# Performance work log

Hardware: AMD Instinct MI355X
Metric: run time of the kernel (lower is better)

## Reference

```python
import jax, jax.numpy as jnp
from jax import lax
import numpy as np

B = 16384


def setup_inputs() -> dict:
    key = jax.random.key(0)
    ks = jax.random.split(key, 8)
    g = lambda k, s: jax.random.normal(k, s, jnp.float32) * 0.05
    return {
        'data': (jax.random.uniform(ks[0], (B, 10, 10, 1)) > 0.9).astype(jnp.float32),
        'w1': g(ks[1], (3, 3, 1, 128)),   'b1': jnp.zeros((128,), jnp.float32),
        'w2': g(ks[2], (3, 3, 128, 128)), 'b2': jnp.zeros((128,), jnp.float32),
        'w3': g(ks[3], (3, 3, 128, 64)),  'b3': jnp.zeros((64,), jnp.float32),
        'w4': g(ks[4], (3, 3, 64, 64)),   'b4': jnp.zeros((64,), jnp.float32),
        'wd1': g(ks[5], (64, 32)), 'bd1': jnp.zeros((32,), jnp.float32),
        'wd2': g(ks[6], (32, 4)),  'bd2': jnp.zeros((4,), jnp.float32),
    }


DN = ('NHWC', 'HWIO', 'NHWC')


def _conv(x, w, b):
    return jax.nn.relu(lax.conv_general_dilated(x, w, (1, 1), 'SAME', dimension_numbers=DN) + b)


def _pool(x):  # MaxPooling2D(pool=2, strides=2, valid)
    return lax.reduce_window(x, -jnp.inf, lax.max, (1, 2, 2, 1), (1, 2, 2, 1), 'VALID')


def reference(data, w1, b1, w2, b2, w3, b3, w4, b4, wd1, bd1, wd2, bd2):
    H = W = 10.0
    x = _pool(_conv(_conv(data, w1, b1), w2, b2))          # [B,5,5,128]
    x = _pool(_conv(_conv(x, w3, b3), w4, b4))             # [B,2,2,64]
    x = jnp.mean(x, axis=(1, 2))                           # GAP -> [B,64]
    x = jax.nn.relu(x @ wd1 + bd1)
    svg = jax.nn.sigmoid(x @ wd2 + bd2).reshape(-1, 2, 2)  # [B,2,2]
    p1 = svg[:, 0, :, None]                                # [B,2,1]
    p2 = svg[:, 1, :, None]
    t = jnp.linspace(0.0, 1.0, 5)
    pts = ((1.0 - t) * p1 + t * p2).transpose(0, 2, 1)     # [B,5,2]
    pts = pts * jnp.array([H, W], jnp.float32)
    # straight-through round
    pts = pts + lax.stop_gradient(jnp.round(pts) - pts)
    # sort by linearized position
    pos = pts[:, :, 0] * W + pts[:, :, 1]
    order = jnp.argsort(pos, axis=1)
    pts = jnp.take_along_axis(pts, order[:, :, None], axis=1)
    # dedup: keep point i if L1 distance to previous point != 0 (first always kept)
    d = jnp.sum(jnp.abs(pts[:, 1:] - pts[:, :-1]), axis=2)           # [B,4]
    d = jnp.concatenate([jnp.ones((d.shape[0], 1), d.dtype), d], 1)  # [B,5]
    keep = d != 0.0
    dest = jnp.where(keep, jnp.cumsum(keep.astype(jnp.int32), axis=1) - 1, 5)
    out = jnp.full((pts.shape[0], 6, 2), -1.0, pts.dtype)  # slot 5 = trash
    out = out.at[jnp.arange(pts.shape[0])[:, None], dest].set(pts)
    return out[:, :5]                                      # [B,5,2], padded with -1
```

## Files before the change

### kernel.cpp

```cpp
#include <hip/hip_runtime.h>
#include <hip/hip_bf16.h>
#include <math.h>

typedef float f4 __attribute__((ext_vector_type(4)));
typedef float f32x4 __attribute__((ext_vector_type(4)));
typedef __bf16 bf16x8 __attribute__((ext_vector_type(8)));
typedef unsigned int uint32x4 __attribute__((ext_vector_type(4)));

#define NT 256

__global__ void repack_w(const float* __restrict__ w1, const float* __restrict__ w2,
                         const float* __restrict__ w3, const float* __restrict__ w4,
                         __hip_bfloat16* __restrict__ ws)
{
    int tid = blockIdx.x * 256 + threadIdx.x;
    const int T2 = 147456, T3 = 73728, T4 = 36864, T1 = 4096;
    if (tid < T2) {
        int j = tid & 7, l = (tid >> 3) & 63, rest = tid >> 9;
        int n = rest & 7, kidx = rest >> 3;
        int cs = kidx & 3, tap = kidx >> 2;
        int ci = cs * 32 + ((l >> 4) << 3) + j;
        int co = (n << 4) + (l & 15);
        ws[tid] = __float2bfloat16(w2[(tap * 128 + ci) * 128 + co]);
    } else if (tid < T2 + T3) {
        int t3 = tid - T2;
        int j = t3 & 7, l = (t3 >> 3) & 63, rest = t3 >> 9;
        int n = rest & 3, kidx = rest >> 2;
        int cs = kidx & 3, tap = kidx >> 2;
        int ci = cs * 32 + ((l >> 4) << 3) + j;
        int co = (n << 4) + (l & 15);
        ws[tid] = __float2bfloat16(w3[(tap * 128 + ci) * 64 + co]);
    } else if (tid < T2 + T3 + T4) {
        int t4 = tid - T2 - T3;
        int j = t4 & 7, l = (t4 >> 3) & 63, rest = t4 >> 9;
        int n = rest & 3, ks = rest >> 2;
        int half = ks & 1, tap = ks >> 1;
        int ci = half * 32 + ((l >> 4) << 3) + j;
        int co = (n << 4) + (l & 15);
        ws[tid] = __float2bfloat16(w4[(tap * 64 + ci) * 64 + co]);
    } else if (tid < T2 + T3 + T4 + T1) {
        int t1 = tid - T2 - T3 - T4;
        int j = t1 & 7, l = (t1 >> 3) & 63, n = (t1 >> 9) & 7;
        int k = ((l >> 4) << 3) + j;
        int co = (n << 4) + (l & 15);
        float v = (k < 9) ? w1[k * 128 + co] : 0.f;
        ws[tid] = __float2bfloat16(v);
    }
}

__global__ __launch_bounds__(NT, 4)
void img2svg_fused(const float* __restrict__ data,
                   const float* __restrict__ b1, const float* __restrict__ b2,
                   const float* __restrict__ b3, const float* __restrict__ b4,
                   const float* __restrict__ wd1, const float* __restrict__ bd1,
                   const float* __restrict__ wd2, const float* __restrict__ bd2,
                   const __hip_bfloat16* __restrict__ wsb,
                   float* __restrict__ out)
{
    __shared__ __align__(16) unsigned char s_u[25856];
    __shared__ float s_in[144];
    __shared__ float s_pool4[4 * 64];
    __shared__ float s_feat[64];
    __shared__ float s_h[32];

    const int t = threadIdx.x;
    const int img = blockIdx.x;
    const int w = t >> 6;
    const int lane = t & 63;
    const int kg = lane >> 4;
    const int l15 = lane & 15;
    const int kgbase1 = kg * 1616;
    const int kgbase2 = kg * 416;

    if (t < 144) {
        int r = t / 12, c = t % 12;
        float v = 0.f;
        if (r >= 1 && r <= 10 && c >= 1 && c <= 10)
            v = data[img * 100 + (r - 1) * 10 + (c - 1)];
        s_in[t] = v;
    }
    if (t < 128)
        *(__bf16*)(s_u + (t >> 3) * 1616 + 1600 + (t & 7) * 2) = (__bf16)0.f;
    s_pool4[t] = 0.f;
    __syncthreads();

    {
        const uint32x4* pk1v = (const uint32x4*)((const __hip_bfloat16*)wsb + 258048);
        uint32x4 B0 = pk1v[((w * 2 + 0) << 6) + lane];
        uint32x4 B1 = pk1v[((w * 2 + 1) << 6) + lane];
        float bj0 = b1[(w * 2 + 0) * 16 + l15];
        float bj1 = b1[(w * 2 + 1) * 16 + l15];
        const int kb0 = (w * 2 + 0) * 2 + (l15 >> 3);
        const int kb1 = (w * 2 + 1) * 2 + (l15 >> 3);
        const int cb = (l15 & 7) * 2;

        for (int mi = 0; mi < 7; ++mi) {
            int p_raw = mi * 16 + l15;
            int p = p_raw < 100 ? p_raw : 99;
            int y = p / 10, x = p - 10 * (p / 10);
            bf16x8 A = __builtin_bit_cast(bf16x8, (uint32x4){0, 0, 0, 0});
            if (kg == 0) {
#pragma unroll
                for (int j = 0; j < 8; ++j)
                    A[j] = (__bf16)s_in[(y + j / 3) * 12 + x + j % 3];
            } else if (kg == 1) {
                A[0] = (__bf16)s_in[(y + 2) * 12 + x + 2];
            }
            f32x4 c0 = (f32x4){bj0, bj0, bj0, bj0};
            f32x4 c1 = (f32x4){bj1, bj1, bj1, bj1};
            c0 = __builtin_amdgcn_mfma_f32_16x16x32_bf16(
                A, __builtin_bit_cast(bf16x8, B0), c0, 0, 0, 0);
            c1 = __builtin_amdgcn_mfma_f32_16x16x32_bf16(
                A, __builtin_bit_cast(bf16x8, B1), c1, 0, 0, 0);
#pragma unroll
            for (int rr = 0; rr < 4; ++rr) {
                int p_out = mi * 16 + kg * 4 + rr;
                if (p_out < 100) {
                    *(__bf16*)(s_u + kb0 * 1616 + p_out * 16 + cb) =
                        (__bf16)fmaxf(c0[rr], 0.f);
                    *(__bf16*)(s_u + kb1 * 1616 + p_out * 16 + cb) =
                        (__bf16)fmaxf(c1[rr], 0.f);
                }
            }
        }
    }
    __syncthreads();

    {
        const int wm = w >> 1, wn = w & 1;
        const uint32x4* pk2v = (const uint32x4*)wsb;

        f32x4 acc[4][4];
#pragma unroll
        for (int j = 0; j < 4; ++j) {
            float bj = b2[wn * 64 + j * 16 + l15];
#pragma unroll
            for (int mi = 0; mi < 4; ++mi) acc[mi][j] = (f32x4){bj, bj, bj, bj};
        }

        int py[4], px[4];
#pragma unroll
        for (int mi = 0; mi < 4; ++mi) {
            int pos = (4 * wm + mi) * 16 + l15;
            py[mi] = pos / 10;
            px[mi] = pos - 10 * py[mi];
        }

        uint32x4 Bc[4], Bn[4];
#pragma unroll
        for (int j = 0; j < 4; ++j) Bc[j] = pk2v[((wn * 4 + j) << 6) + lane];

        for (int tap = 0; tap < 9; ++tap) {
            const int dy = tap / 3, dx = tap - 3 * (tap / 3);
            int ao[4];
#pragma unroll
            for (int mi = 0; mi < 4; ++mi) {
                int ay = py[mi] + dy - 1, ax = px[mi] + dx - 1;
                int r = ((unsigned)ay < 10u && (unsigned)ax < 10u) ? ay * 10 + ax : 100;
                ao[mi] = (r << 4) + kgbase1;
            }
#pragma unroll
            for (int cs = 0; cs < 4; ++cs) {
                int nk = tap * 4 + cs + 1;
                if (nk < 36) {
#pragma unroll
                    for (int j = 0; j < 4; ++j)
                        Bn[j] = pk2v[(((nk << 3) + wn * 4 + j) << 6) + lane];
                }
                bf16x8 A[4];
#pragma unroll
                for (int mi = 0; mi < 4; ++mi)
                    A[mi] = *(const bf16x8*)(const void*)(s_u + cs * 6464 + ao[mi]);
#pragma unroll
                for (int mi = 0; mi < 4; ++mi)
#pragma unroll
                    for (int j = 0; j < 4; ++j)
                        acc[mi][j] = __builtin_amdgcn_mfma_f32_16x16x32_bf16(
                            A[mi], __builtin_bit_cast(bf16x8, Bc[j]), acc[mi][j], 0, 0, 0);
#pragma unroll
                for (int j = 0; j < 4; ++j) Bc[j] = Bn[j];
            }
        }
        __syncthreads();

        float* p2f = (float*)s_u;
        for (int i = t; i < 3200; i += NT) p2f[i] = 0.f;
        if (t < 128)
            *(__bf16*)(s_u + 13312 + (t >> 3) * 416 + 400 + (t & 7) * 2) = (__bf16)0.f;
        if (t < 64)
            *(__bf16*)(s_u + 19968 + (t >> 3) * 416 + 400 + (t & 7) * 2) = (__bf16)0.f;
        __syncthreads();

#pragma unroll
        for (int mi = 0; mi < 4; ++mi) {
            int posb = (4 * wm + mi) * 16 + kg * 4;
#pragma unroll
            for (int j = 0; j < 4; ++j) {
                int co = wn * 64 + j * 16 + l15;
                float m01 = fmaxf(fmaxf(acc[mi][j][0], acc[mi][j][1]), 0.f);
                float m23 = fmaxf(fmaxf(acc[mi][j][2], acc[mi][j][3]), 0.f);
                if (posb < 100) {
                    int y = posb / 10, x = posb - 10 * (posb / 10);
                    atomicMax((int*)&p2f[(((y >> 1) * 5 + (x >> 1)) << 7) + co],
                              __float_as_int(m01));
                }
                int pos2 = posb + 2;
                if (pos2 < 100) {
                    int y = pos2 / 10, x = pos2 - 10 * (pos2 / 10);
                    atomicMax((int*)&p2f[(((y >> 1) * 5 + (x >> 1)) << 7) + co],
                              __float_as_int(m23));
                }
            }
        }
    }
    __syncthreads();

    {
        const float* p2f = (const float*)s_u;
        for (int i = t; i < 3200; i += NT) {
            int r = i >> 7, c = i & 127;
            float v = p2f[i];
            *(__bf16*)(s_u + 13312 + (c >> 3) * 416 + (r << 4) + (c & 7) * 2) = (__bf16)v;
        }
    }
    __syncthreads();

    {
        const int mt = w & 1, ntp = w >> 1;
        const uint32x4* pk3v = (const uint32x4*)((const __hip_bfloat16*)wsb + 147456);

        f32x4 c3[2];
#pragma unroll
        for (int j = 0; j < 2; ++j) {
            float bj = b3[ntp * 32 + j * 16 + l15];
            c3[j] = (f32x4){bj, bj, bj, bj};
        }
        int pos = mt * 16 + l15;
        int p3y = pos / 5, p3x = pos - 5 * (pos / 5);

        uint32x4 Bc[2], Bn[2];
#pragma unroll
        for (int j = 0; j < 2; ++j) Bc[j] = pk3v[((ntp * 2 + j) << 6) + lane];

        for (int tap = 0; tap < 9; ++tap) {
            const int dy = tap / 3, dx = tap - 3 * (tap / 3);
            int ay = p3y + dy - 1, ax = p3x + dx - 1;
            int r = ((unsigned)ay < 5u && (unsigned)ax < 5u) ? ay * 5 + ax : 25;
            int ao = 13312 + (r << 4) + kgbase2;
#pragma unroll
            for (int cs = 0; cs < 4; ++cs) {
                int nk = tap * 4 + cs + 1;
                if (nk < 36) {
#pragma unroll
                    for (int j = 0; j < 2; ++j)
                        Bn[j] = pk3v[(((nk << 2) + ntp * 2 + j) << 6) + lane];
                }
                bf16x8 A = *(const bf16x8*)(const void*)(s_u + cs * 1664 + ao);
#pragma unroll
                for (int j = 0; j < 2; ++j)
                    c3[j] = __builtin_amdgcn_mfma_f32_16x16x32_bf16(
                        A, __builtin_bit_cast(bf16x8, Bc[j]), c3[j], 0, 0, 0);
#pragma unroll
                for (int j = 0; j < 2; ++j) Bc[j] = Bn[j];
            }
        }
#pragma unroll
        for (int j = 0; j < 2; ++j) {
            int co = ntp * 32 + j * 16 + l15;
            int kb = co >> 3, cb = (co & 7) * 2;
#pragma unroll
            for (int rr = 0; rr < 4; ++rr) {
                int p = mt * 16 + kg * 4 + rr;
                if (p < 25)
                    *(__bf16*)(s_u + 19968 + kb * 416 + p * 16 + cb) =
                        (__bf16)fmaxf(c3[j][rr], 0.f);
            }
        }
    }
    __syncthreads();

    {
        const int nt = w;
        const uint32x4* pk4v = (const uint32x4*)((const __hip_bfloat16*)wsb + 221184);
        float bj = b4[nt * 16 + l15];
        f32x4 c4 = (f32x4){bj, bj, bj, bj};
        int py = l15 >> 2, px = l15 & 3;

        uint32x4 Bc = pk4v[(nt << 6) + lane], Bn;
        for (int ks = 0; ks < 18; ++ks) {
            if (ks < 17) Bn = pk4v[((((ks + 1) << 2) + nt) << 6) + lane];
            int half = ks & 1, tap = ks >> 1;
            int dy = tap / 3, dx = tap - 3 * (tap / 3);
            int ay = py + dy - 1, ax = px + dx - 1;
            int r = ((unsigned)ay < 5u && (unsigned)ax < 5u) ? ay * 5 + ax : 25;
            bf16x8 A = *(const bf16x8*)(const void*)(
                s_u + 19968 + (half * 4 + kg) * 416 + (r << 4));
            c4 = __builtin_amdgcn_mfma_f32_16x16x32_bf16(
                A, __builtin_bit_cast(bf16x8, Bc), c4, 0, 0, 0);
            Bc = Bn;
        }
#pragma unroll
        for (int rr = 0; rr < 4; ++rr) {
            int p = kg * 4 + rr;
            int cell = ((p >> 2) >> 1) * 2 + ((p & 3) >> 1);
            float rv = fmaxf(c4[rr], 0.f);
            atomicMax((int*)&s_pool4[cell * 64 + nt * 16 + l15], __float_as_int(rv));
        }
    }
    __syncthreads();

    if (t < 64) {
        float f = 0.25f * (s_pool4[t] + s_pool4[64 + t] + s_pool4[128 + t] + s_pool4[192 + t]);
        s_feat[t] = f;
    }
    __syncthreads();
    if (t < 32) {
        float h = bd1[t];
        for (int i = 0; i < 64; ++i) h = fmaf(s_feat[i], wd1[i * 32 + t], h);
        s_h[t] = fmaxf(h, 0.f);
    }
    __syncthreads();

    if (t == 0) {
        float v[4];
#pragma unroll
        for (int o = 0; o < 4; ++o) {
            float vv = bd2[o];
            for (int i = 0; i < 32; ++i) vv = fmaf(s_h[i], wd2[i * 4 + o], vv);
            v[o] = 1.f / (1.f + expf(-vv));
        }
        float px[5], py[5], pp[5];
#pragma unroll
        for (int k = 0; k < 5; ++k) {
            float tk = 0.25f * (float)k;
            float gx = ((1.f - tk) * v[0] + tk * v[2]) * 10.f;
            float gy = ((1.f - tk) * v[1] + tk * v[3]) * 10.f;
            px[k] = rintf(gx);
            py[k] = rintf(gy);
            pp[k] = px[k] * 10.f + py[k];
        }
#pragma unroll
        for (int pass = 0; pass < 4; ++pass)
#pragma unroll
            for (int i = 0; i < 4 - pass; ++i) {
                bool sw = pp[i] > pp[i + 1];
                float a, b;
                a = pp[i]; b = pp[i + 1]; pp[i] = sw ? b : a; pp[i + 1] = sw ? a : b;
                a = px[i]; b = px[i + 1]; px[i] = sw ? b : a; px[i + 1] = sw ? a : b;
                a = py[i]; b = py[i + 1]; py[i] = sw ? b : a; py[i + 1] = sw ? a : b;
            }
        float* op = out + img * 10;
#pragma unroll
        for (int i = 0; i < 5; ++i) { op[2 * i] = -1.f; op[2 * i + 1] = -1.f; }
        int k2 = 0;
#pragma unroll
        for (int i = 0; i < 5; ++i) {
            bool keep;
            if (i == 0) keep = true;
            else keep = (fabsf(px[i] - px[i - 1]) + fabsf(py[i] - py[i - 1])) != 0.f;
            if (keep) {
                op[2 * k2] = px[i];
                op[2 * k2 + 1] = py[i];
                ++k2;
            }
        }
    }
}

extern "C" void kernel_launch(void* const* d_in, const int* in_sizes, int n_in,
                              void* d_out, int out_size, void* d_ws, size_t ws_size,
                              hipStream_t stream) {
    const float* data = (const float*)d_in[0];
    const float* w1  = (const float*)d_in[1];
    const float* b1  = (const float*)d_in[2];
    const float* w2  = (const float*)d_in[3];
    const float* b2  = (const float*)d_in[4];
    const float* w3  = (const float*)d_in[5];
    const float* b3  = (const float*)d_in[6];
    const float* w4  = (const float*)d_in[7];
    const float* b4  = (const float*)d_in[8];
    const float* wd1 = (const float*)d_in[9];
    const float* bd1 = (const float*)d_in[10];
    const float* wd2 = (const float*)d_in[11];
    const float* bd2 = (const float*)d_in[12];
    float* out = (float*)d_out;
    __hip_bfloat16* wsb = (__hip_bfloat16*)d_ws;

    repack_w<<<1024, 256, 0, stream>>>(w1, w2, w3, w4, wsb);

    int nimg = in_sizes[0] / 100;
    img2svg_fused<<<nimg, NT, 0, stream>>>(data, b1, b2, b3, b4,
                                           wd1, bd1, wd2, bd2, wsb, out);
}
```

Baseline: 675.0 us.

## Repartition conv2 waves over output channels and replace pooling atomics with two-stage max

Conv2 now splits work so each wave owns 32 output channels across all 7 position tiles, where before waves used a 2x2 split over positions and channels. Each weight fragment is loaded once per k-step per wave, and the register prefetch double-buffer is dropped. The 2x2 max-pool no longer zero-inits shared memory and uses atomicMax. Horizontal pairs are maxed in registers and written plainly, and the vertical max is fused into the bf16 transpose pass. Shared memory grows to hold the unpooled row buffer, which may lower occupancy, and the loss of weight prefetch may expose global load latency.

```diff
diff --git a/kernel.cpp b/kernel.cpp
--- a/kernel.cpp
+++ b/kernel.cpp
@@ -57,7 +57,7 @@
                    const __hip_bfloat16* __restrict__ wsb,
                    float* __restrict__ out)
 {
-    __shared__ __align__(16) unsigned char s_u[25856];
+    __shared__ __align__(16) unsigned char s_u[32256];
     __shared__ float s_in[144];
     __shared__ float s_pool4[4 * 64];
     __shared__ float s_feat[64];
@@ -127,105 +127,87 @@
     __syncthreads();
 
     {
-        const int wm = w >> 1, wn = w & 1;
         const uint32x4* pk2v = (const uint32x4*)wsb;
 
-        f32x4 acc[4][4];
-#pragma unroll
-        for (int j = 0; j < 4; ++j) {
-            float bj = b2[wn * 64 + j * 16 + l15];
-#pragma unroll
-            for (int mi = 0; mi < 4; ++mi) acc[mi][j] = (f32x4){bj, bj, bj, bj};
-        }
-
-        int py[4], px[4];
-#pragma unroll
-        for (int mi = 0; mi < 4; ++mi) {
-            int pos = (4 * wm + mi) * 16 + l15;
+        f32x4 acc[7][2];
+#pragma unroll
+        for (int j = 0; j < 2; ++j) {
+            float bj = b2[(w * 2 + j) * 16 + l15];
+#pragma unroll
+            for (int mi = 0; mi < 7; ++mi) acc[mi][j] = (f32x4){bj, bj, bj, bj};
+        }
+
+        int py[7], px[7];
+#pragma unroll
+        for (int mi = 0; mi < 7; ++mi) {
+            int pos = mi * 16 + l15;
             py[mi] = pos / 10;
             px[mi] = pos - 10 * py[mi];
         }
 
-        uint32x4 Bc[4], Bn[4];
-#pragma unroll
-        for (int j = 0; j < 4; ++j) Bc[j] = pk2v[((wn * 4 + j) << 6) + lane];
-
         for (int tap = 0; tap < 9; ++tap) {
             const int dy = tap / 3, dx = tap - 3 * (tap / 3);
-            int ao[4];
-#pragma unroll
-            for (int mi = 0; mi < 4; ++mi) {
+            int ao[7];
+#pragma unroll
+            for (int mi = 0; mi < 7; ++mi) {
                 int ay = py[mi] + dy - 1, ax = px[mi] + dx - 1;
                 int r = ((unsigned)ay < 10u && (unsigned)ax < 10u) ? ay * 10 + ax : 100;
                 ao[mi] = (r << 4) + kgbase1;
             }
 #pragma unroll
             for (int cs = 0; cs < 4; ++cs) {
-                int nk = tap * 4 + cs + 1;
-                if (nk < 36) {
-#pragma unroll
-                    for (int j = 0; j < 4; ++j)
-                        Bn[j] = pk2v[(((nk << 3) + wn * 4 + j) << 6) + lane];
+                int ks = tap * 4 + cs;
+                uint32x4 Bc0 = pk2v[(((ks << 3) + w * 2 + 0) << 6) + lane];
+                uint32x4 Bc1 = pk2v[(((ks << 3) + w * 2 + 1) << 6) + lane];
+#pragma unroll
+                for (int mi = 0; mi < 7; ++mi) {
+                    bf16x8 A = *(const bf16x8*)(const void*)(s_u + cs * 6464 + ao[mi]);
+                    acc[mi][0] = __builtin_amdgcn_mfma_f32_16x16x32_bf16(
+                        A, __builtin_bit_cast(bf16x8, Bc0), acc[mi][0], 0, 0, 0);
+                    acc[mi][1] = __builtin_amdgcn_mfma_f32_16x16x32_bf16(
+                        A, __builtin_bit_cast(bf16x8, Bc1), acc[mi][1], 0, 0, 0);
                 }
-                bf16x8 A[4];
-#pragma unroll
-                for (int mi = 0; mi < 4; ++mi)
-                    A[mi] = *(const bf16x8*)(const void*)(s_u + cs * 6464 + ao[mi]);
-#pragma unroll
-                for (int mi = 0; mi < 4; ++mi)
-#pragma unroll
-                    for (int j = 0; j < 4; ++j)
-                        acc[mi][j] = __builtin_amdgcn_mfma_f32_16x16x32_bf16(
-                            A[mi], __builtin_bit_cast(bf16x8, Bc[j]), acc[mi][j], 0, 0, 0);
-#pragma unroll
-                for (int j = 0; j < 4; ++j) Bc[j] = Bn[j];
             }
         }
         __syncthreads();
 
-        float* p2f = (float*)s_u;
-        for (int i = t; i < 3200; i += NT) p2f[i] = 0.f;
-        if (t < 128)
-            *(__bf16*)(s_u + 13312 + (t >> 3) * 416 + 400 + (t & 7) * 2) = (__bf16)0.f;
-        if (t < 64)
-            *(__bf16*)(s_u + 19968 + (t >> 3) * 416 + 400 + (t & 7) * 2) = (__bf16)0.f;
-        __syncthreads();
-
-#pragma unroll
-        for (int mi = 0; mi < 4; ++mi) {
-            int posb = (4 * wm + mi) * 16 + kg * 4;
-#pragma unroll
-            for (int j = 0; j < 4; ++j) {
-                int co = wn * 64 + j * 16 + l15;
-                float m01 = fmaxf(fmaxf(acc[mi][j][0], acc[mi][j][1]), 0.f);
-                float m23 = fmaxf(fmaxf(acc[mi][j][2], acc[mi][j][3]), 0.f);
-                if (posb < 100) {
-                    int y = posb / 10, x = posb - 10 * (posb / 10);
-                    atomicMax((int*)&p2f[(((y >> 1) * 5 + (x >> 1)) << 7) + co],
-                              __float_as_int(m01));
+        float* xp = (float*)s_u;
+#pragma unroll
+        for (int mi = 0; mi < 7; ++mi) {
+            int posb = mi * 16 + kg * 4;
+            if (mi < 6 || kg == 0) {
+                int s = posb >> 1;
+#pragma unroll
+                for (int j = 0; j < 2; ++j) {
+                    int co = (w * 2 + j) * 16 + l15;
+                    float m01 = fmaxf(fmaxf(acc[mi][j][0], acc[mi][j][1]), 0.f);
+                    float m23 = fmaxf(fmaxf(acc[mi][j][2], acc[mi][j][3]), 0.f);
+                    xp[s * 128 + co] = m01;
+                    xp[(s + 1) * 128 + co] = m23;
                 }
-                int pos2 = posb + 2;
-                if (pos2 < 100) {
-                    int y = pos2 / 10, x = pos2 - 10 * (pos2 / 10);
-                    atomicMax((int*)&p2f[(((y >> 1) * 5 + (x >> 1)) << 7) + co],
-                              __float_as_int(m23));
-                }
-            }
-        }
-    }
-    __syncthreads();
-
-    {
-        const float* p2f = (const float*)s_u;
+            }
+        }
+    }
+    __syncthreads();
+
+    {
+        const float* xp = (const float*)s_u;
         for (int i = t; i < 3200; i += NT) {
             int r = i >> 7, c = i & 127;
-            float v = p2f[i];
-            *(__bf16*)(s_u + 13312 + (c >> 3) * 416 + (r << 4) + (c & 7) * 2) = (__bf16)v;
-        }
-    }
-    __syncthreads();
-
-    {
+            int y2 = r / 5, x2 = r - 5 * y2;
+            int s = y2 * 10 + x2;
+            float v = fmaxf(xp[s * 128 + c], xp[(s + 5) * 128 + c]);
+            *(__bf16*)(s_u + 25600 + (c >> 3) * 416 + (r << 4) + (c & 7) * 2) = (__bf16)v;
+        }
+        if (t < 128)
+            *(__bf16*)(s_u + 25600 + (t >> 3) * 416 + 400 + (t & 7) * 2) = (__bf16)0.f;
+    }
+    __syncthreads();
+
+    {
+        if (t < 64)
+            *(__bf16*)(s_u + (t >> 3) * 416 + 400 + (t & 7) * 2) = (__bf16)0.f;
+
         const int mt = w & 1, ntp = w >> 1;
         const uint32x4* pk3v = (const uint32x4*)((const __hip_bfloat16*)wsb + 147456);
 
@@ -246,7 +228,7 @@
             const int dy = tap / 3, dx = tap - 3 * (tap / 3);
             int ay = p3y + dy - 1, ax = p3x + dx - 1;
             int r = ((unsigned)ay < 5u && (unsigned)ax < 5u) ? ay * 5 + ax : 25;
-            int ao = 13312 + (r << 4) + kgbase2;
+            int ao = 25600 + (r << 4) + kgbase2;
 #pragma unroll
             for (int cs = 0; cs < 4; ++cs) {
                 int nk = tap * 4 + cs + 1;
@@ -272,7 +254,7 @@
             for (int rr = 0; rr < 4; ++rr) {
                 int p = mt * 16 + kg * 4 + rr;
                 if (p < 25)
-                    *(__bf16*)(s_u + 19968 + kb * 416 + p * 16 + cb) =
+                    *(__bf16*)(s_u + kb * 416 + p * 16 + cb) =
                         (__bf16)fmaxf(c3[j][rr], 0.f);
             }
         }
@@ -294,7 +276,7 @@
             int ay = py + dy - 1, ax = px + dx - 1;
             int r = ((unsigned)ay < 5u && (unsigned)ax < 5u) ? ay * 5 + ax : 25;
             bf16x8 A = *(const bf16x8*)(const void*)(
-                s_u + 19968 + (half * 4 + kg) * 416 + (r << 4));
+                s_u + (half * 4 + kg) * 416 + (r << 4));
             c4 = __builtin_amdgcn_mfma_f32_16x16x32_bf16(
                 A, __builtin_bit_cast(bf16x8, Bc), c4, 0, 0, 0);
             Bc = Bn;
```

After: 611.7 us. 9.4% less time.
